# Kernel optimization log

Hardware: AMD Instinct MI355X
Metric: run time of the kernel (lower is better)

Reference implementation:

```python
import jax, jax.numpy as jnp
import numpy as np

T, B, C, H, L = 384, 48, 256, 256, 2


def setup_inputs() -> dict:
    key = jax.random.key(0)
    ks = jax.random.split(key, 8)
    s = 1.0 / np.sqrt(H)  # torch GRUCell uniform(-1/sqrt(H), 1/sqrt(H)) init
    xav = np.sqrt(2.0 / (H + 1))  # xavier_normal_ for the [1,H] skip-gate linear
    return {
        "x": jax.random.normal(ks[0], (T, B, C), jnp.float32),
        "hiddens": jax.random.normal(ks[1], (L, 1, H), jnp.float32),
        "w_ih": jax.random.uniform(ks[2], (L, 3 * H, C), jnp.float32, -s, s),
        "w_hh": jax.random.uniform(ks[3], (L, 3 * H, H), jnp.float32, -s, s),
        "b_ih": jax.random.uniform(ks[4], (L, 3 * H), jnp.float32, -s, s),
        "b_hh": jax.random.uniform(ks[5], (L, 3 * H), jnp.float32, -s, s),
        "lw": jax.random.normal(ks[6], (L, 1, H), jnp.float32) * xav,
        "lb": jnp.ones((L, 1), jnp.float32),  # linear.bias.data.fill_(1)
    }


def _ste(v):
    # straight-through round: forward round, backward identity
    return v + jax.lax.stop_gradient(jnp.round(v) - v)


def reference(x, hiddens, w_ih, w_hh, b_ih, b_hh, lw, lb):
    Tn, Bn, _ = x.shape
    Ln, _, Hn = hiddens.shape
    skip = jnp.zeros((Bn,), dtype=bool)          # carried across layers (as in torch loop)
    du = jnp.zeros((Bn, 1), x.dtype)             # delta_u, carried across layers
    inp = x
    hs, bus = [], []
    for i in range(Ln):
        wi, wh, bi, bh = w_ih[i], w_hh[i], b_ih[i], b_hh[i]
        lwi, lbi = lw[i], lb[i]
        h0 = jnp.broadcast_to(hiddens[i], (Bn, Hn))  # h.repeat(1, bs, 1)
        u0 = jnp.ones((Bn, 1), x.dtype)              # u reset per layer

        def step(carry, x_t):
            h, u, skp, d = carry
            bu = _ste(u)                                  # [B,1]
            # GRUCell: gates order (r, z, n)
            gi = x_t @ wi.T + bi                          # [B,3H]
            gh = h @ wh.T + bh                            # [B,3H]
            i_r, i_z, i_n = jnp.split(gi, 3, axis=1)
            h_r, h_z, h_n = jnp.split(gh, 3, axis=1)
            r = jax.nn.sigmoid(i_r + h_r)
            z = jax.nn.sigmoid(i_z + h_z)
            n = jnp.tanh(i_n + r * h_n)
            cand = (1.0 - z) * n + z * h
            # non-skip branch
            h_ns = cand * bu
            d_ns = jax.nn.sigmoid(h_ns @ lwi.T + lbi)     # [B,1]
            s = skp[:, None]
            new_h = jnp.where(s, h * (1.0 - bu), h_ns)
            new_d = jnp.where(s, d, d_ns)
            new_u = jnp.where(s, jnp.clip(u + d, 0.0, 1.0) * (1.0 - bu), d_ns * bu)
            # n_skips_after = ceil(0.5/new_u) - 1 ; skip if > 0 (non-diff path)
            nsa = jnp.ceil(0.5 / jax.lax.stop_gradient(new_u)) - 1.0
            new_skip = nsa[:, 0] > 0
            return (new_h, new_u, new_skip, new_d), (new_h, bu)

        (h_f, _, skip, du), (ys, bu_seq) = jax.lax.scan(step, (h0, u0, skip, du), inp)
        inp = ys                 # [T,B,H] feeds next layer
        hs.append(h_f)           # final hidden [B,H]
        bus.append(bu_seq)       # [T,B,1]
    out = inp
    hs = jnp.stack(hs, axis=0)                                   # [L,B,H]
    total_u = jnp.concatenate([b[:, :, 0].T for b in bus], 1)    # [B, L*T]
    return (out, hs, total_u)
```

## Files before the change

### kernel.cpp

```cpp
#include <hip/hip_runtime.h>
#include <stdint.h>


#define T_STEPS 384
#define BATCH   48
#define HID     256

__device__ __forceinline__ float sigm_(float x) { return 1.f / (1.f + __expf(-x)); }
__device__ __forceinline__ float tanh_(float x) {
    float ax = fabsf(x);
    float e  = __expf(-2.f * ax);
    float r  = (1.f - e) / (1.f + e);
    return copysignf(r, x);
}

__global__ __launch_bounds__(256, 2) void gemm_nt(const float* __restrict__ X,
                                                  const float* __restrict__ W,
                                                  const float* __restrict__ B,
                                                  float* __restrict__ O)
{
    __shared__ float As[32 * 140];
    __shared__ float Bs[32 * 68];

    const int tid = threadIdx.x;
    const int tx  = tid & 15;
    const int ty  = tid >> 4;
    const int n0  = blockIdx.x * 64;
    const int m0  = blockIdx.y * 128;

    float acc[8][4];
#pragma unroll
    for (int i = 0; i < 8; ++i)
#pragma unroll
        for (int j = 0; j < 4; ++j) acc[i][j] = 0.f;

    const float4 bias4 = *reinterpret_cast<const float4*>(B + n0 + tx * 4);

    for (int kc = 0; kc < 8; ++kc) {
        const int k0 = kc * 32;
        float4 a[4], bb[2];
#pragma unroll
        for (int j = 0; j < 4; ++j) {
            int f = tid + 256 * j, r = f >> 3, cq = f & 7;
            a[j] = *reinterpret_cast<const float4*>(X + (size_t)(m0 + r) * 256 + k0 + cq * 4);
        }
#pragma unroll
        for (int j = 0; j < 2; ++j) {
            int f = tid + 256 * j, r = f >> 3, cq = f & 7;
            bb[j] = *reinterpret_cast<const float4*>(W + (size_t)(n0 + r) * 256 + k0 + cq * 4);
        }
        __syncthreads();
#pragma unroll
        for (int j = 0; j < 4; ++j) {
            int f = tid + 256 * j, r = f >> 3, cq = f & 7;
            As[(cq * 4 + 0) * 140 + r] = a[j].x;
            As[(cq * 4 + 1) * 140 + r] = a[j].y;
            As[(cq * 4 + 2) * 140 + r] = a[j].z;
            As[(cq * 4 + 3) * 140 + r] = a[j].w;
        }
#pragma unroll
        for (int j = 0; j < 2; ++j) {
            int f = tid + 256 * j, r = f >> 3, cq = f & 7;
            Bs[(cq * 4 + 0) * 68 + r] = bb[j].x;
            Bs[(cq * 4 + 1) * 68 + r] = bb[j].y;
            Bs[(cq * 4 + 2) * 68 + r] = bb[j].z;
            Bs[(cq * 4 + 3) * 68 + r] = bb[j].w;
        }
        __syncthreads();
#pragma unroll 8
        for (int kk = 0; kk < 32; ++kk) {
            float4 av0 = *reinterpret_cast<const float4*>(As + kk * 140 + ty * 8);
            float4 av1 = *reinterpret_cast<const float4*>(As + kk * 140 + ty * 8 + 4);
            float4 bv  = *reinterpret_cast<const float4*>(Bs + kk * 68 + tx * 4);
            float am[8] = {av0.x, av0.y, av0.z, av0.w, av1.x, av1.y, av1.z, av1.w};
            float bn[4] = {bv.x, bv.y, bv.z, bv.w};
#pragma unroll
            for (int i = 0; i < 8; ++i)
#pragma unroll
                for (int j = 0; j < 4; ++j) acc[i][j] = fmaf(am[i], bn[j], acc[i][j]);
        }
    }
#pragma unroll
    for (int i = 0; i < 8; ++i) {
        int row = m0 + ty * 8 + i;
        float4 o;
        o.x = acc[i][0] + bias4.x;
        o.y = acc[i][1] + bias4.y;
        o.z = acc[i][2] + bias4.z;
        o.w = acc[i][3] + bias4.w;
        *reinterpret_cast<float4*>(O + (size_t)row * 768 + n0 + tx * 4) = o;
    }
}

__global__ __launch_bounds__(512, 2) void rec_layer(
    const float* __restrict__ GI, float* __restrict__ Yout,
    const float* __restrict__ whh, const float* __restrict__ bhh,
    const float* __restrict__ lwl, const float* __restrict__ lbl,
    const float* __restrict__ hid,
    unsigned long long* XH, unsigned long long* PD,
    float* __restrict__ hsout, float* __restrict__ tuout)
{
    __shared__ float hbuf[2112];
    __shared__ float pdw[2][8];

    const int tid  = threadIdx.x;
    const int lane = tid & 63;
    const int w    = tid >> 6;
    const int g    = lane & 15;
    const int s    = lane >> 4;
    const int b    = blockIdx.x % 48;
    const int p    = blockIdx.x / 48;
    const int q    = 1 - p;
    const int c    = p * 128 + w * 16 + g;

    float4 WrO[8], WzO[8], WnO[8], WrP[8], WzP[8], WnP[8];
    {
        const size_t rR = (size_t)c * 256;
        const size_t rZ = (size_t)(256 + c) * 256;
        const size_t rN = (size_t)(512 + c) * 256;
        const int ko = p * 128 + s * 32;
        const int kq = q * 128 + s * 32;
        const float4* a = reinterpret_cast<const float4*>(whh + rR + ko);
        const float4* bv = reinterpret_cast<const float4*>(whh + rZ + ko);
        const float4* cv = reinterpret_cast<const float4*>(whh + rN + ko);
        const float4* d4 = reinterpret_cast<const float4*>(whh + rR + kq);
        const float4* e4 = reinterpret_cast<const float4*>(whh + rZ + kq);
        const float4* f4 = reinterpret_cast<const float4*>(whh + rN + kq);
#pragma unroll
        for (int i = 0; i < 8; ++i) {
            WrO[i] = a[i];  WzO[i] = bv[i]; WnO[i] = cv[i];
            WrP[i] = d4[i]; WzP[i] = e4[i]; WnP[i] = f4[i];
        }
    }

    const float bhr = bhh[c], bhz = bhh[256 + c], bhn = bhh[512 + c];
    const float lwc = lwl[c];
    const float lbv = lbl[0];

    if (tid < 256) {
        float v = hid[tid];
        hbuf[tid] = v; hbuf[264 + tid] = v; hbuf[528 + tid] = v; hbuf[792 + tid] = v;
    }
    __syncthreads();

    float gir, giz, gin;
    {
        const size_t g0 = (size_t)b * 768 + c;
        gir = GI[g0]; giz = GI[g0 + 256]; gin = GI[g0 + 512];
    }
    float sAr, sAz, sAn;
    {
        float ar = 0.f, az = 0.f, an = 0.f;
        const float4* ho = reinterpret_cast<const float4*>(hbuf + s * 264 + p * 128 + s * 32);
        const float4* hq = reinterpret_cast<const float4*>(hbuf + s * 264 + q * 128 + s * 32);
#pragma unroll
        for (int i = 0; i < 8; ++i) {
            float4 hv = ho[i];
            ar = fmaf(WrO[i].x, hv.x, ar); ar = fmaf(WrO[i].y, hv.y, ar);
            ar = fmaf(WrO[i].z, hv.z, ar); ar = fmaf(WrO[i].w, hv.w, ar);
            az = fmaf(WzO[i].x, hv.x, az); az = fmaf(WzO[i].y, hv.y, az);
            az = fmaf(WzO[i].z, hv.z, az); az = fmaf(WzO[i].w, hv.w, az);
            an = fmaf(WnO[i].x, hv.x, an); an = fmaf(WnO[i].y, hv.y, an);
            an = fmaf(WnO[i].z, hv.z, an); an = fmaf(WnO[i].w, hv.w, an);
        }
#pragma unroll
        for (int i = 0; i < 8; ++i) {
            float4 hv = hq[i];
            ar = fmaf(WrP[i].x, hv.x, ar); ar = fmaf(WrP[i].y, hv.y, ar);
            ar = fmaf(WrP[i].z, hv.z, ar); ar = fmaf(WrP[i].w, hv.w, ar);
            az = fmaf(WzP[i].x, hv.x, az); az = fmaf(WzP[i].y, hv.y, az);
            az = fmaf(WzP[i].z, hv.z, az); az = fmaf(WzP[i].w, hv.w, az);
            an = fmaf(WnP[i].x, hv.x, an); an = fmaf(WnP[i].y, hv.y, an);
            an = fmaf(WnP[i].z, hv.z, an); an = fmaf(WnP[i].w, hv.w, an);
        }
        ar += __shfl_xor(ar, 16); ar += __shfl_xor(ar, 32);
        az += __shfl_xor(az, 16); az += __shfl_xor(az, 32);
        an += __shfl_xor(an, 16); an += __shfl_xor(an, 32);
        sAr = ar; sAz = az; sAn = an;
    }

    float u = 1.f, d = 0.f;
    bool  skip = false;
    int   ns = 0;
    int   hp = 0;

    unsigned long long* XHb = XH + b * 512;
    unsigned long long* PDb = PD + b * 4;

    for (int t = 0; t < T_STEPS; ++t) {
        const float bu  = rintf(u);
        const float obu = 1.f - bu;
        const size_t yrow = ((size_t)t * 48 + b) * 256;
        const int tp = (t < T_STEPS - 1) ? t + 1 : t;
        const size_t gpb = ((size_t)tp * 48 + b) * 768 + c;

        if (skip) {
            float* hb = hbuf + hp * 1056;
            if (s == 0) {
                float hcv = hb[c];
                float nh  = hcv * obu;
                if (bu != 0.f) { hb[c] = nh; hb[264 + c] = nh; hb[528 + c] = nh; hb[792 + c] = nh; }
                Yout[yrow + c] = nh;
                if (t == T_STEPS - 1) hsout[b * 256 + c] = nh;
            }
            if (bu != 0.f) { sAr = 0.f; sAz = 0.f; sAn = 0.f; }
            if (p == 0 && tid == 0) tuout[b * 768 + t] = bu;
            float pr = GI[gpb], pz = GI[gpb + 256], pn = GI[gpb + 512];
            u    = fminf(fmaxf(u + d, 0.f), 1.f) * obu;
            skip = (u < 0.5f);
            __syncthreads();
            gir = pr; giz = pz; gin = pn;
        } else {
            const int sl = ns & 1;
            const unsigned int tag = (unsigned int)ns + 1u;

            float hcv = hbuf[hp * 1056 + s * 264 + c];
            float rr  = sigm_(gir + sAr + bhr);
            float zz  = sigm_(giz + sAz + bhz);
            float tn  = tanh_(gin + rr * (sAn + bhn));
            float nh  = ((1.f - zz) * tn + zz * hcv) * bu;
            float pdv = nh * lwc;

            float* hbn = hbuf + (hp ^ 1) * 1056;
            if (s == 0) {
                unsigned long long pk0 = ((unsigned long long)tag << 32) |
                                         (unsigned long long)__float_as_uint(nh);
                __hip_atomic_store(XHb + sl * 256 + c, pk0, __ATOMIC_RELAXED, __HIP_MEMORY_SCOPE_AGENT);
                hbn[c] = nh; hbn[264 + c] = nh; hbn[528 + c] = nh; hbn[792 + c] = nh;
                Yout[yrow + c] = nh;
                if (t == T_STEPS - 1) hsout[b * 256 + c] = nh;
            }
            pdv += __shfl_xor(pdv, 1);  pdv += __shfl_xor(pdv, 2);  pdv += __shfl_xor(pdv, 4);
            pdv += __shfl_xor(pdv, 8);  pdv += __shfl_xor(pdv, 16); pdv += __shfl_xor(pdv, 32);
            pdv *= 0.25f;
            if (lane == 0) pdw[sl][w] = pdv;
            if (p == 0 && tid == 0) tuout[b * 768 + t] = bu;
            __syncthreads();

            float ownpd = ((pdw[sl][0] + pdw[sl][1]) + (pdw[sl][2] + pdw[sl][3]))
                        + ((pdw[sl][4] + pdw[sl][5]) + (pdw[sl][6] + pdw[sl][7]));
            if (tid == 0) {
                unsigned long long pk0 = ((unsigned long long)tag << 32) |
                                         (unsigned long long)__float_as_uint(ownpd);
                __hip_atomic_store(PDb + sl * 2 + p, pk0, __ATOMIC_RELAXED, __HIP_MEMORY_SCOPE_AGENT);
            }

            unsigned long long pk = 0;
            if (tid < 128)
                pk = __hip_atomic_load(XHb + sl * 256 + q * 128 + tid, __ATOMIC_RELAXED, __HIP_MEMORY_SCOPE_AGENT);
            float pr = GI[gpb], pz = GI[gpb + 256], pn = GI[gpb + 512];

            float ar = 0.f, az = 0.f, an = 0.f;
            {
                const float4* ho = reinterpret_cast<const float4*>(hbn + s * 264 + p * 128 + s * 32);
#pragma unroll
                for (int i = 0; i < 8; ++i) {
                    float4 hv = ho[i];
                    ar = fmaf(WrO[i].x, hv.x, ar); ar = fmaf(WrO[i].y, hv.y, ar);
                    ar = fmaf(WrO[i].z, hv.z, ar); ar = fmaf(WrO[i].w, hv.w, ar);
                    az = fmaf(WzO[i].x, hv.x, az); az = fmaf(WzO[i].y, hv.y, az);
                    az = fmaf(WzO[i].z, hv.z, az); az = fmaf(WzO[i].w, hv.w, az);
                    an = fmaf(WnO[i].x, hv.x, an); an = fmaf(WnO[i].y, hv.y, an);
                    an = fmaf(WnO[i].z, hv.z, an); an = fmaf(WnO[i].w, hv.w, an);
                }
            }
            if (tid < 128) {
                while ((unsigned int)(pk >> 32) < tag)
                    pk = __hip_atomic_load(XHb + sl * 256 + q * 128 + tid, __ATOMIC_RELAXED, __HIP_MEMORY_SCOPE_AGENT);
                float v = __uint_as_float((unsigned int)pk);
                int qc = q * 128 + tid;
                hbn[qc] = v; hbn[264 + qc] = v; hbn[528 + qc] = v; hbn[792 + qc] = v;
            }
            __syncthreads();

            unsigned long long pkq = __hip_atomic_load(PDb + sl * 2 + q, __ATOMIC_RELAXED, __HIP_MEMORY_SCOPE_AGENT);

            {
                const float4* hq = reinterpret_cast<const float4*>(hbn + s * 264 + q * 128 + s * 32);
#pragma unroll
                for (int i = 0; i < 8; ++i) {
                    float4 hv = hq[i];
                    ar = fmaf(WrP[i].x, hv.x, ar); ar = fmaf(WrP[i].y, hv.y, ar);
                    ar = fmaf(WrP[i].z, hv.z, ar); ar = fmaf(WrP[i].w, hv.w, ar);
                    az = fmaf(WzP[i].x, hv.x, az); az = fmaf(WzP[i].y, hv.y, az);
                    az = fmaf(WzP[i].z, hv.z, az); az = fmaf(WzP[i].w, hv.w, az);
                    an = fmaf(WnP[i].x, hv.x, an); an = fmaf(WnP[i].y, hv.y, an);
                    an = fmaf(WnP[i].z, hv.z, an); an = fmaf(WnP[i].w, hv.w, an);
                }
            }
            ar += __shfl_xor(ar, 16); ar += __shfl_xor(ar, 32);
            az += __shfl_xor(az, 16); az += __shfl_xor(az, 32);
            an += __shfl_xor(an, 16); an += __shfl_xor(an, 32);
            sAr = ar; sAz = az; sAn = an;

            while ((unsigned int)(pkq >> 32) < tag)
                pkq = __hip_atomic_load(PDb + sl * 2 + q, __ATOMIC_RELAXED, __HIP_MEMORY_SCOPE_AGENT);
            const float pdq = __uint_as_float((unsigned int)pkq);

            float dns = sigm_((ownpd + pdq) + lbv);
            u = dns * bu; d = dns;
            skip = (u < 0.5f);
            ns++; hp ^= 1;
            gir = pr; giz = pz; gin = pn;
        }
    }
}

extern "C" void kernel_launch(void* const* d_in, const int* in_sizes, int n_in,
                              void* d_out, int out_size, void* d_ws, size_t ws_size,
                              hipStream_t stream)
{
    const float* x   = (const float*)d_in[0];
    const float* hid = (const float*)d_in[1];
    const float* wih = (const float*)d_in[2];
    const float* whh = (const float*)d_in[3];
    const float* bih = (const float*)d_in[4];
    const float* bhh = (const float*)d_in[5];
    const float* lw  = (const float*)d_in[6];
    const float* lb  = (const float*)d_in[7];
    float* out = (float*)d_out;

    float* ws = (float*)d_ws;
    float* GI = ws;
    float* Y0 = GI + (size_t)18432 * 768;
    unsigned long long* XH0 = (unsigned long long*)(Y0 + (size_t)18432 * 256);
    unsigned long long* XH1 = XH0 + 48 * 512;
    unsigned long long* PD0 = XH1 + 48 * 512;
    unsigned long long* PD1 = PD0 + 48 * 4;

    float* OUTy = out;
    float* HS   = out + (size_t)18432 * 256;
    float* TU   = HS + 2 * 48 * 256;

    hipMemsetAsync(XH0, 0, (size_t)(48 * 512 * 2 + 48 * 4 * 2) * sizeof(unsigned long long), stream);

    dim3 ggrid(12, 144), gblk(256);
    gemm_nt<<<ggrid, gblk, 0, stream>>>(x, wih, bih, GI);
    rec_layer<<<96, 512, 0, stream>>>(GI, Y0, whh, bhh, lw, lb, hid, XH0, PD0, HS, TU);
    gemm_nt<<<ggrid, gblk, 0, stream>>>(Y0, wih + 196608, bih + 768, GI);
    rec_layer<<<96, 512, 0, stream>>>(GI, OUTy, whh + 196608, bhh + 768, lw + 256, lb + 1,
                                      hid + 256, XH1, PD1, HS + 12288, TU + 384);
}
```

Measured before the change: 2.033 ms.

## Add fast-path mirrored flag buffers and lighter barriers to cross-block recurrence handoff

```diff
diff --git a/kernel.cpp b/kernel.cpp
--- a/kernel.cpp
+++ b/kernel.cpp
@@ -12,6 +12,17 @@
     float e  = __expf(-2.f * ax);
     float r  = (1.f - e) / (1.f + e);
     return copysignf(r, x);
+}
+
+__device__ __forceinline__ void bar_lds() {
+    asm volatile("s_waitcnt lgkmcnt(0)\n\ts_barrier" ::: "memory");
+}
+
+__device__ __forceinline__ unsigned long long ld_l2(const unsigned long long* p) {
+    unsigned long long v;
+    asm volatile("global_load_dwordx2 %0, %1, off sc0\n\ts_waitcnt vmcnt(0)"
+                 : "=v"(v) : "v"(p) : "memory");
+    return v;
 }
 
 __global__ __launch_bounds__(256, 2) void gemm_nt(const float* __restrict__ X,
@@ -97,7 +108,8 @@
     const float* __restrict__ whh, const float* __restrict__ bhh,
     const float* __restrict__ lwl, const float* __restrict__ lbl,
     const float* __restrict__ hid,
-    unsigned long long* XH, unsigned long long* PD,
+    unsigned long long* XH, unsigned long long* XF,
+    unsigned long long* PD, unsigned long long* PF,
     float* __restrict__ hsout, float* __restrict__ tuout)
 {
     __shared__ float hbuf[2112];
@@ -120,7 +132,7 @@
         const size_t rN = (size_t)(512 + c) * 256;
         const int ko = p * 128 + s * 32;
         const int kq = q * 128 + s * 32;
-        const float4* a = reinterpret_cast<const float4*>(whh + rR + ko);
+        const float4* a  = reinterpret_cast<const float4*>(whh + rR + ko);
         const float4* bv = reinterpret_cast<const float4*>(whh + rZ + ko);
         const float4* cv = reinterpret_cast<const float4*>(whh + rN + ko);
         const float4* d4 = reinterpret_cast<const float4*>(whh + rR + kq);
@@ -141,7 +153,7 @@
         float v = hid[tid];
         hbuf[tid] = v; hbuf[264 + tid] = v; hbuf[528 + tid] = v; hbuf[792 + tid] = v;
     }
-    __syncthreads();
+    bar_lds();
 
     float gir, giz, gin;
     {
@@ -185,7 +197,9 @@
     int   hp = 0;
 
     unsigned long long* XHb = XH + b * 512;
+    unsigned long long* XFb = XF + b * 512;
     unsigned long long* PDb = PD + b * 4;
+    unsigned long long* PFb = PF + b * 4;
 
     for (int t = 0; t < T_STEPS; ++t) {
         const float bu  = rintf(u);
@@ -193,6 +207,8 @@
         const size_t yrow = ((size_t)t * 48 + b) * 256;
         const int tp = (t < T_STEPS - 1) ? t + 1 : t;
         const size_t gpb = ((size_t)tp * 48 + b) * 768 + c;
+
+        float pr = GI[gpb], pz = GI[gpb + 256], pn = GI[gpb + 512];
 
         if (skip) {
             float* hb = hbuf + hp * 1056;
@@ -205,11 +221,9 @@
             }
             if (bu != 0.f) { sAr = 0.f; sAz = 0.f; sAn = 0.f; }
             if (p == 0 && tid == 0) tuout[b * 768 + t] = bu;
-            float pr = GI[gpb], pz = GI[gpb + 256], pn = GI[gpb + 512];
             u    = fminf(fmaxf(u + d, 0.f), 1.f) * obu;
             skip = (u < 0.5f);
-            __syncthreads();
-            gir = pr; giz = pz; gin = pn;
+            bar_lds();
         } else {
             const int sl = ns & 1;
             const unsigned int tag = (unsigned int)ns + 1u;
@@ -223,9 +237,10 @@
 
             float* hbn = hbuf + (hp ^ 1) * 1056;
             if (s == 0) {
-                unsigned long long pk0 = ((unsigned long long)tag << 32) |
-                                         (unsigned long long)__float_as_uint(nh);
-                __hip_atomic_store(XHb + sl * 256 + c, pk0, __ATOMIC_RELAXED, __HIP_MEMORY_SCOPE_AGENT);
+                unsigned long long pk = ((unsigned long long)tag << 32) |
+                                        (unsigned long long)__float_as_uint(nh);
+                __hip_atomic_store(XHb + sl * 256 + c, pk, __ATOMIC_RELAXED, __HIP_MEMORY_SCOPE_AGENT);
+                *(volatile unsigned long long*)(XFb + sl * 256 + c) = pk;
                 hbn[c] = nh; hbn[264 + c] = nh; hbn[528 + c] = nh; hbn[792 + c] = nh;
                 Yout[yrow + c] = nh;
                 if (t == T_STEPS - 1) hsout[b * 256 + c] = nh;
@@ -235,20 +250,22 @@
             pdv *= 0.25f;
             if (lane == 0) pdw[sl][w] = pdv;
             if (p == 0 && tid == 0) tuout[b * 768 + t] = bu;
-            __syncthreads();
+
+            unsigned long long pk0 = 0;
+            if (tid < 128)
+                pk0 = __hip_atomic_load(XHb + sl * 256 + q * 128 + tid, __ATOMIC_RELAXED, __HIP_MEMORY_SCOPE_AGENT);
+
+            bar_lds();
 
             float ownpd = ((pdw[sl][0] + pdw[sl][1]) + (pdw[sl][2] + pdw[sl][3]))
                         + ((pdw[sl][4] + pdw[sl][5]) + (pdw[sl][6] + pdw[sl][7]));
             if (tid == 0) {
-                unsigned long long pk0 = ((unsigned long long)tag << 32) |
-                                         (unsigned long long)__float_as_uint(ownpd);
-                __hip_atomic_store(PDb + sl * 2 + p, pk0, __ATOMIC_RELAXED, __HIP_MEMORY_SCOPE_AGENT);
-            }
-
-            unsigned long long pk = 0;
-            if (tid < 128)
-                pk = __hip_atomic_load(XHb + sl * 256 + q * 128 + tid, __ATOMIC_RELAXED, __HIP_MEMORY_SCOPE_AGENT);
-            float pr = GI[gpb], pz = GI[gpb + 256], pn = GI[gpb + 512];
+                unsigned long long pk = ((unsigned long long)tag << 32) |
+                                        (unsigned long long)__float_as_uint(ownpd);
+                __hip_atomic_store(PDb + sl * 2 + p, pk, __ATOMIC_RELAXED, __HIP_MEMORY_SCOPE_AGENT);
+                *(volatile unsigned long long*)(PFb + sl * 2 + p) = pk;
+            }
+            unsigned long long pkq = __hip_atomic_load(PDb + sl * 2 + q, __ATOMIC_RELAXED, __HIP_MEMORY_SCOPE_AGENT);
 
             float ar = 0.f, az = 0.f, an = 0.f;
             {
@@ -265,15 +282,20 @@
                 }
             }
             if (tid < 128) {
-                while ((unsigned int)(pk >> 32) < tag)
-                    pk = __hip_atomic_load(XHb + sl * 256 + q * 128 + tid, __ATOMIC_RELAXED, __HIP_MEMORY_SCOPE_AGENT);
-                float v = __uint_as_float((unsigned int)pk);
-                int qc = q * 128 + tid;
+                const int qc = q * 128 + tid;
+                const unsigned long long* fap = XFb + sl * 256 + qc;
+                const unsigned long long* slp = XHb + sl * 256 + qc;
+                while ((unsigned int)(pk0 >> 32) < tag) {
+                    pk0 = ld_l2(fap);
+                    if ((unsigned int)(pk0 >> 32) >= tag) break;
+                    pk0 = ld_l2(fap);
+                    if ((unsigned int)(pk0 >> 32) >= tag) break;
+                    pk0 = __hip_atomic_load(slp, __ATOMIC_RELAXED, __HIP_MEMORY_SCOPE_AGENT);
+                }
+                float v = __uint_as_float((unsigned int)pk0);
                 hbn[qc] = v; hbn[264 + qc] = v; hbn[528 + qc] = v; hbn[792 + qc] = v;
             }
-            __syncthreads();
-
-            unsigned long long pkq = __hip_atomic_load(PDb + sl * 2 + q, __ATOMIC_RELAXED, __HIP_MEMORY_SCOPE_AGENT);
+            bar_lds();
 
             {
                 const float4* hq = reinterpret_cast<const float4*>(hbn + s * 264 + q * 128 + s * 32);
@@ -293,16 +315,25 @@
             an += __shfl_xor(an, 16); an += __shfl_xor(an, 32);
             sAr = ar; sAz = az; sAn = an;
 
-            while ((unsigned int)(pkq >> 32) < tag)
-                pkq = __hip_atomic_load(PDb + sl * 2 + q, __ATOMIC_RELAXED, __HIP_MEMORY_SCOPE_AGENT);
+            {
+                const unsigned long long* fap = PFb + sl * 2 + q;
+                const unsigned long long* slp = PDb + sl * 2 + q;
+                while ((unsigned int)(pkq >> 32) < tag) {
+                    pkq = ld_l2(fap);
+                    if ((unsigned int)(pkq >> 32) >= tag) break;
+                    pkq = ld_l2(fap);
+                    if ((unsigned int)(pkq >> 32) >= tag) break;
+                    pkq = __hip_atomic_load(slp, __ATOMIC_RELAXED, __HIP_MEMORY_SCOPE_AGENT);
+                }
+            }
             const float pdq = __uint_as_float((unsigned int)pkq);
 
             float dns = sigm_((ownpd + pdq) + lbv);
             u = dns * bu; d = dns;
             skip = (u < 0.5f);
             ns++; hp ^= 1;
-            gir = pr; giz = pz; gin = pn;
-        }
+        }
+        gir = pr; giz = pz; gin = pn;
     }
 }
 
@@ -325,19 +356,24 @@
     float* Y0 = GI + (size_t)18432 * 768;
     unsigned long long* XH0 = (unsigned long long*)(Y0 + (size_t)18432 * 256);
     unsigned long long* XH1 = XH0 + 48 * 512;
-    unsigned long long* PD0 = XH1 + 48 * 512;
-    unsigned long long* PD1 = PD0 + 48 * 4;
+    unsigned long long* XF0 = XH1 + 48 * 512;
+    unsigned long long* XF1 = XF0 + 48 * 512;
+    unsigned long long* PD0 = XF1 + 48 * 512;
+    unsigned long long* PD1 = PD0 + 192;
+    unsigned long long* PF0 = PD1 + 192;
+    unsigned long long* PF1 = PF0 + 192;
 
     float* OUTy = out;
     float* HS   = out + (size_t)18432 * 256;
     float* TU   = HS + 2 * 48 * 256;
 
-    hipMemsetAsync(XH0, 0, (size_t)(48 * 512 * 2 + 48 * 4 * 2) * sizeof(unsigned long long), stream);
+    hipMemsetAsync(XH0, 0, (size_t)99072 * sizeof(unsigned long long), stream);
 
     dim3 ggrid(12, 144), gblk(256);
     gemm_nt<<<ggrid, gblk, 0, stream>>>(x, wih, bih, GI);
-    rec_layer<<<96, 512, 0, stream>>>(GI, Y0, whh, bhh, lw, lb, hid, XH0, PD0, HS, TU);
+    rec_layer<<<96, 512, 0, stream>>>(GI, Y0, whh, bhh, lw, lb, hid,
+                                      XH0, XF0, PD0, PF0, HS, TU);
     gemm_nt<<<ggrid, gblk, 0, stream>>>(Y0, wih + 196608, bih + 768, GI);
     rec_layer<<<96, 512, 0, stream>>>(GI, OUTy, whh + 196608, bhh + 768, lw + 256, lb + 1,
-                                      hid + 256, XH1, PD1, HS + 12288, TU + 384);
-}
+                                      hid + 256, XH1, XF1, PD1, PF1, HS + 12288, TU + 384);
+}
```

After: 3.228 ms. +58.8%, slower.

## Compute peer skip-gate dot locally and drop separate PD cross-block handshake

Applied to the files above, without the earlier changes.

```diff
diff --git a/kernel.cpp b/kernel.cpp
--- a/kernel.cpp
+++ b/kernel.cpp
@@ -12,6 +12,10 @@
     float e  = __expf(-2.f * ax);
     float r  = (1.f - e) / (1.f + e);
     return copysignf(r, x);
+}
+
+__device__ __forceinline__ void bar_lds() {
+    asm volatile("s_waitcnt lgkmcnt(0)\n\ts_barrier" ::: "memory");
 }
 
 __global__ __launch_bounds__(256, 2) void gemm_nt(const float* __restrict__ X,
@@ -97,11 +101,12 @@
     const float* __restrict__ whh, const float* __restrict__ bhh,
     const float* __restrict__ lwl, const float* __restrict__ lbl,
     const float* __restrict__ hid,
-    unsigned long long* XH, unsigned long long* PD,
+    unsigned long long* XH,
     float* __restrict__ hsout, float* __restrict__ tuout)
 {
     __shared__ float hbuf[2112];
-    __shared__ float pdw[2][8];
+    __shared__ float pdw[8];
+    __shared__ float qpd[8];
 
     const int tid  = threadIdx.x;
     const int lane = tid & 63;
@@ -120,7 +125,7 @@
         const size_t rN = (size_t)(512 + c) * 256;
         const int ko = p * 128 + s * 32;
         const int kq = q * 128 + s * 32;
-        const float4* a = reinterpret_cast<const float4*>(whh + rR + ko);
+        const float4* a  = reinterpret_cast<const float4*>(whh + rR + ko);
         const float4* bv = reinterpret_cast<const float4*>(whh + rZ + ko);
         const float4* cv = reinterpret_cast<const float4*>(whh + rN + ko);
         const float4* d4 = reinterpret_cast<const float4*>(whh + rR + kq);
@@ -136,12 +141,13 @@
     const float bhr = bhh[c], bhz = bhh[256 + c], bhn = bhh[512 + c];
     const float lwc = lwl[c];
     const float lbv = lbl[0];
+    const float lwq = (tid < 128) ? lwl[q * 128 + tid] : 0.f;
 
     if (tid < 256) {
         float v = hid[tid];
         hbuf[tid] = v; hbuf[264 + tid] = v; hbuf[528 + tid] = v; hbuf[792 + tid] = v;
     }
-    __syncthreads();
+    bar_lds();
 
     float gir, giz, gin;
     {
@@ -185,7 +191,6 @@
     int   hp = 0;
 
     unsigned long long* XHb = XH + b * 512;
-    unsigned long long* PDb = PD + b * 4;
 
     for (int t = 0; t < T_STEPS; ++t) {
         const float bu  = rintf(u);
@@ -195,6 +200,7 @@
         const size_t gpb = ((size_t)tp * 48 + b) * 768 + c;
 
         if (skip) {
+            float pr = GI[gpb], pz = GI[gpb + 256], pn = GI[gpb + 512];
             float* hb = hbuf + hp * 1056;
             if (s == 0) {
                 float hcv = hb[c];
@@ -205,14 +211,18 @@
             }
             if (bu != 0.f) { sAr = 0.f; sAz = 0.f; sAn = 0.f; }
             if (p == 0 && tid == 0) tuout[b * 768 + t] = bu;
-            float pr = GI[gpb], pz = GI[gpb + 256], pn = GI[gpb + 512];
             u    = fminf(fmaxf(u + d, 0.f), 1.f) * obu;
             skip = (u < 0.5f);
-            __syncthreads();
+            bar_lds();
             gir = pr; giz = pz; gin = pn;
         } else {
             const int sl = ns & 1;
             const unsigned int tag = (unsigned int)ns + 1u;
+
+            unsigned long long pk0 = 0;
+            if (tid < 128)
+                pk0 = __hip_atomic_load(XHb + sl * 256 + q * 128 + tid, __ATOMIC_RELAXED, __HIP_MEMORY_SCOPE_AGENT);
+            float pr = GI[gpb], pz = GI[gpb + 256], pn = GI[gpb + 512];
 
             float hcv = hbuf[hp * 1056 + s * 264 + c];
             float rr  = sigm_(gir + sAr + bhr);
@@ -223,9 +233,9 @@
 
             float* hbn = hbuf + (hp ^ 1) * 1056;
             if (s == 0) {
-                unsigned long long pk0 = ((unsigned long long)tag << 32) |
-                                         (unsigned long long)__float_as_uint(nh);
-                __hip_atomic_store(XHb + sl * 256 + c, pk0, __ATOMIC_RELAXED, __HIP_MEMORY_SCOPE_AGENT);
+                unsigned long long pk = ((unsigned long long)tag << 32) |
+                                        (unsigned long long)__float_as_uint(nh);
+                __hip_atomic_store(XHb + sl * 256 + c, pk, __ATOMIC_RELAXED, __HIP_MEMORY_SCOPE_AGENT);
                 hbn[c] = nh; hbn[264 + c] = nh; hbn[528 + c] = nh; hbn[792 + c] = nh;
                 Yout[yrow + c] = nh;
                 if (t == T_STEPS - 1) hsout[b * 256 + c] = nh;
@@ -233,22 +243,13 @@
             pdv += __shfl_xor(pdv, 1);  pdv += __shfl_xor(pdv, 2);  pdv += __shfl_xor(pdv, 4);
             pdv += __shfl_xor(pdv, 8);  pdv += __shfl_xor(pdv, 16); pdv += __shfl_xor(pdv, 32);
             pdv *= 0.25f;
-            if (lane == 0) pdw[sl][w] = pdv;
+            if (lane == 0) pdw[w] = pdv;
             if (p == 0 && tid == 0) tuout[b * 768 + t] = bu;
-            __syncthreads();
-
-            float ownpd = ((pdw[sl][0] + pdw[sl][1]) + (pdw[sl][2] + pdw[sl][3]))
-                        + ((pdw[sl][4] + pdw[sl][5]) + (pdw[sl][6] + pdw[sl][7]));
-            if (tid == 0) {
-                unsigned long long pk0 = ((unsigned long long)tag << 32) |
-                                         (unsigned long long)__float_as_uint(ownpd);
-                __hip_atomic_store(PDb + sl * 2 + p, pk0, __ATOMIC_RELAXED, __HIP_MEMORY_SCOPE_AGENT);
-            }
-
-            unsigned long long pk = 0;
-            if (tid < 128)
-                pk = __hip_atomic_load(XHb + sl * 256 + q * 128 + tid, __ATOMIC_RELAXED, __HIP_MEMORY_SCOPE_AGENT);
-            float pr = GI[gpb], pz = GI[gpb + 256], pn = GI[gpb + 512];
+
+            bar_lds();
+
+            float ownpd = ((pdw[0] + pdw[1]) + (pdw[2] + pdw[3]))
+                        + ((pdw[4] + pdw[5]) + (pdw[6] + pdw[7]));
 
             float ar = 0.f, az = 0.f, an = 0.f;
             {
@@ -265,15 +266,21 @@
                 }
             }
             if (tid < 128) {
-                while ((unsigned int)(pk >> 32) < tag)
-                    pk = __hip_atomic_load(XHb + sl * 256 + q * 128 + tid, __ATOMIC_RELAXED, __HIP_MEMORY_SCOPE_AGENT);
-                float v = __uint_as_float((unsigned int)pk);
-                int qc = q * 128 + tid;
+                const int qc = q * 128 + tid;
+                const unsigned long long* slp = XHb + sl * 256 + qc;
+                while ((unsigned int)(pk0 >> 32) < tag)
+                    pk0 = __hip_atomic_load(slp, __ATOMIC_RELAXED, __HIP_MEMORY_SCOPE_AGENT);
+                float v = __uint_as_float((unsigned int)pk0);
                 hbn[qc] = v; hbn[264 + qc] = v; hbn[528 + qc] = v; hbn[792 + qc] = v;
-            }
-            __syncthreads();
-
-            unsigned long long pkq = __hip_atomic_load(PDb + sl * 2 + q, __ATOMIC_RELAXED, __HIP_MEMORY_SCOPE_AGENT);
+                float pq = v * lwq;
+                pq += __shfl_xor(pq, 1); pq += __shfl_xor(pq, 2);
+                pq += __shfl_xor(pq, 4); pq += __shfl_xor(pq, 8);
+                if ((lane & 15) == 0) qpd[tid >> 4] = pq;
+            }
+            bar_lds();
+
+            float pdq = ((qpd[0] + qpd[1]) + (qpd[2] + qpd[3]))
+                      + ((qpd[4] + qpd[5]) + (qpd[6] + qpd[7]));
 
             {
                 const float4* hq = reinterpret_cast<const float4*>(hbn + s * 264 + q * 128 + s * 32);
@@ -292,10 +299,6 @@
             az += __shfl_xor(az, 16); az += __shfl_xor(az, 32);
             an += __shfl_xor(an, 16); an += __shfl_xor(an, 32);
             sAr = ar; sAz = az; sAn = an;
-
-            while ((unsigned int)(pkq >> 32) < tag)
-                pkq = __hip_atomic_load(PDb + sl * 2 + q, __ATOMIC_RELAXED, __HIP_MEMORY_SCOPE_AGENT);
-            const float pdq = __uint_as_float((unsigned int)pkq);
 
             float dns = sigm_((ownpd + pdq) + lbv);
             u = dns * bu; d = dns;
@@ -325,19 +328,17 @@
     float* Y0 = GI + (size_t)18432 * 768;
     unsigned long long* XH0 = (unsigned long long*)(Y0 + (size_t)18432 * 256);
     unsigned long long* XH1 = XH0 + 48 * 512;
-    unsigned long long* PD0 = XH1 + 48 * 512;
-    unsigned long long* PD1 = PD0 + 48 * 4;
 
     float* OUTy = out;
     float* HS   = out + (size_t)18432 * 256;
     float* TU   = HS + 2 * 48 * 256;
 
-    hipMemsetAsync(XH0, 0, (size_t)(48 * 512 * 2 + 48 * 4 * 2) * sizeof(unsigned long long), stream);
+    hipMemsetAsync(XH0, 0, (size_t)(2 * 48 * 512) * sizeof(unsigned long long), stream);
 
     dim3 ggrid(12, 144), gblk(256);
     gemm_nt<<<ggrid, gblk, 0, stream>>>(x, wih, bih, GI);
-    rec_layer<<<96, 512, 0, stream>>>(GI, Y0, whh, bhh, lw, lb, hid, XH0, PD0, HS, TU);
+    rec_layer<<<96, 512, 0, stream>>>(GI, Y0, whh, bhh, lw, lb, hid, XH0, HS, TU);
     gemm_nt<<<ggrid, gblk, 0, stream>>>(Y0, wih + 196608, bih + 768, GI);
     rec_layer<<<96, 512, 0, stream>>>(GI, OUTy, whh + 196608, bhh + 768, lw + 256, lb + 1,
-                                      hid + 256, XH1, PD1, HS + 12288, TU + 384);
-}
+                                      hid + 256, XH1, HS + 12288, TU + 384);
+}
```

Result: slower. 2.782 ms (+36.8%).
